# Kernel tuning notes

Hardware: AMD Instinct MI355X
Metric: run time of the kernel (lower is better)

The kernel has to match this reference:

```python
import jax, jax.numpy as jnp
import numpy as np

FAR = 10.0
RAST = 256          # rast_size default
ORIG_W, ORIG_H = 256.0, 256.0  # orig_size default
CHUNK = 32          # faces processed per scan step
EPS = 1e-9


def _project(vertices, K, R, t, dist):
    # persp projection with lens distortion; vertices [B,V,3] -> [B,V,3] (u,v in [-1,1], z depth)
    v = jnp.einsum('bvj,bij->bvi', vertices, R) + t
    x, y, z = v[..., 0], v[..., 1], v[..., 2]
    x_ = x / (z + EPS)
    y_ = y / (z + EPS)
    k1, k2, p1, p2, k3 = (dist[:, None, i] for i in range(5))
    r2 = x_ * x_ + y_ * y_  # == r**2 in original (r = sqrt(x_^2+y_^2))
    radial = 1.0 + k1 * r2 + k2 * r2 ** 2 + k3 * r2 ** 3
    x__ = x_ * radial + 2.0 * p1 * x_ * y_ + p2 * (r2 + 2.0 * x_ ** 2)
    y__ = y_ * radial + p1 * (r2 + 2.0 * y_ ** 2) + 2.0 * p2 * x_ * y_
    pts = jnp.stack([x__, y__, jnp.ones_like(z)], axis=-1)
    pts = jnp.einsum('bvj,bij->bvi', pts, K)
    u, vv = pts[..., 0], pts[..., 1]
    vv = ORIG_H - vv
    u = 2.0 * (u - ORIG_W / 2.0) / ORIG_W
    vv = 2.0 * (vv - ORIG_H / 2.0) / ORIG_H
    return jnp.stack([u, vv, z], axis=-1)


def _rasterize(fverts):
    # fverts: [B,F,3,3] per-face screen-space vertices (u,v,z). Z-buffer depth raster + coverage mask.
    B, F = fverts.shape[0], fverts.shape[1]
    pad = (-F) % CHUNK
    fv = jnp.pad(fverts, ((0, 0), (0, pad), (0, 0), (0, 0)))  # padded faces are degenerate (den==0)
    nc = (F + pad) // CHUNK
    fv = fv.reshape(B, nc, CHUNK, 3, 3).transpose(1, 0, 2, 3, 4)  # [nc,B,CHUNK,3,3]
    # pixel centers in [-1,1]; row i top-to-bottom maps to y = -1..1 (consistent with flipped v)
    g = 2.0 * (jnp.arange(RAST, dtype=jnp.float32) + 0.5) / RAST - 1.0
    X = g[None, None, None, :]   # cols
    Y = g[None, None, :, None]   # rows

    def body(carry, ch):
        zbuf, cover = carry
        e = lambda i, j: ch[:, :, i, j][:, :, None, None]
        ax, ay, az = e(0, 0), e(0, 1), e(0, 2)
        bx, by, bz = e(1, 0), e(1, 1), e(1, 2)
        cx, cy, cz = e(2, 0), e(2, 1), e(2, 2)
        den = (bx - ax) * (cy - ay) - (by - ay) * (cx - ax)
        ok = jnp.abs(den) > 1e-8
        den_s = jnp.where(ok, den, 1.0)
        # barycentric coords of each pixel wrt this face (signed; fill_back provides both windings)
        w0 = ((by - cy) * (X - cx) + (cx - bx) * (Y - cy)) / den_s
        w1 = ((cy - ay) * (X - cx) + (ax - cx) * (Y - cy)) / den_s
        w2 = 1.0 - w0 - w1
        zs = lambda zz: jnp.where(zz > 1e-8, zz, 1.0)
        inv = w0 / zs(az) + w1 / zs(bz) + w2 / zs(cz)  # perspective-correct 1/z interp
        valid = ok & (w0 >= 0) & (w1 >= 0) & (w2 >= 0)
        valid = valid & (az > 1e-8) & (bz > 1e-8) & (cz > 1e-8) & (inv > 1e-8)
        zp = 1.0 / jnp.where(valid, inv, 1.0)
        zc = jnp.min(jnp.where(valid, zp, FAR), axis=1)  # nearest face in this chunk [B,S,S]
        return (jnp.minimum(zbuf, zc), cover | jnp.any(valid, axis=1)), None

    zbuf0 = jnp.full((B, RAST, RAST), FAR, dtype=jnp.float32)
    cov0 = jnp.zeros((B, RAST, RAST), dtype=bool)
    (zbuf, cover), _ = jax.lax.scan(body, (zbuf0, cov0), fv)
    return zbuf, cover


def _normalize_depth(img, far):
    img_inf = (img == far).astype(jnp.float32)
    img_no_back = (1.0 - img_inf) * img
    img_max = img_no_back.max(axis=1, keepdims=True).max(axis=2, keepdims=True)
    img_min = img.min(axis=1, keepdims=True).min(axis=2, keepdims=True)
    nd = (img_max - img) / (img_max - img_min + 1e-4)
    return jnp.clip(nd, 0.0, 1.0)


def _forward(vertices, faces, intr, R, t, dist_coeffs):
    # fill_back=True: append faces with reversed vertex order
    faces_fb = jnp.concatenate([faces, faces[:, :, ::-1]], axis=1)
    uvz = _project(vertices, intr, R, t, dist_coeffs)
    fverts = jax.vmap(lambda v, f: v[f])(uvz, faces_fb)  # [B,F,3,3]
    zbuf, cover = _rasterize(fverts)
    dep = _normalize_depth(zbuf, FAR)
    mask = cover.astype(jnp.float32)
    return dep, mask


def setup_inputs():
    key = jax.random.key(0)
    k0, k1, k2 = jax.random.split(key, 3)
    B, V, F = 4, 778, 1538  # MANO hand mesh
    vertices = jax.random.normal(k0, (B, V, 3), dtype=jnp.float32) * 0.1 \
        + jnp.array([0.0, 0.0, 0.6], dtype=jnp.float32)  # blob 0.6m in front of camera
    faces = jax.random.randint(k1, (B, F, 3), 0, V, dtype=jnp.int32)
    K = jnp.tile(jnp.array([[500.0, 0.0, 128.0],
                            [0.0, 500.0, 128.0],
                            [0.0, 0.0, 1.0]], dtype=jnp.float32)[None], (B, 1, 1))
    R = jnp.tile(jnp.eye(3, dtype=jnp.float32)[None], (B, 1, 1))
    t = jnp.zeros((B, 1, 3), dtype=jnp.float32)
    dist_coeffs = jax.random.uniform(k2, (B, 5), dtype=jnp.float32) * 0.01
    return {"vertices": vertices, "faces": faces, "intr": K, "R": R, "t": t,
            "dist_coeffs": dist_coeffs}


def reference(vertices, faces, intr, R, t, dist_coeffs):
    return _forward(vertices, faces, intr, R, t, dist_coeffs)
```

## Files before the change

kernel.cpp:

```cpp
#include <hip/hip_runtime.h>
#include <cstdint>

#define RASTN 256
#define FARV 10.0f
#define FARBITS 0x41200000u
#define SPLIT 4
#define NBUCK 1024
#define NINITY 8

__device__ __forceinline__ float gval(int i) {
    return (2.0f * ((float)i + 0.5f)) / 256.0f - 1.0f;
}

__global__ __launch_bounds__(1024) void prep_sort_kernel(
    const float* __restrict__ verts, const int* __restrict__ faces,
    const float* __restrict__ Km, const float* __restrict__ Rm,
    const float* __restrict__ tm, const float* __restrict__ dm,
    float4* __restrict__ rec, uint2* __restrict__ sax, unsigned short* __restrict__ stri,
    unsigned int* __restrict__ zbits, unsigned int* __restrict__ mm,
    float* __restrict__ uvzg, int V, int F, int F2, int B, int npix)
{
#pragma clang fp contract(off)
    __shared__ float s_uvz[1024*3];
    __shared__ unsigned int s_pk[4096];
    __shared__ unsigned short s_bk[4096];
    __shared__ unsigned int s_hist[NBUCK], s_cnt2[NBUCK];
    __shared__ unsigned int s_ws[16];
    int b = blockIdx.x, y = blockIdx.y, tid = threadIdx.x;
    int lane = tid & 63, wv16 = tid >> 6;
    uint4* zb4 = (uint4*)(zbits + (size_t)b * npix);
    int n4 = npix >> 2;
    int sl0 = (n4 * y) / NINITY, sl1 = (n4 * (y + 1)) / NINITY;
    for (int i = sl0 + tid; i < sl1; i += 1024)
        zb4[i] = make_uint4(FARBITS, FARBITS, FARBITS, FARBITS);
    if (y > 0) return;
    if (tid == 0) { mm[2*b] = 0u; mm[2*b+1] = FARBITS; }
    for (int i = tid; i < NBUCK; i += 1024) s_hist[i] = 0u;
    bool inlds = (V <= 1024);
    const float* R = Rm + b*9; const float* K = Km + b*9;
    const float* t = tm + b*3; const float* d = dm + b*5;
    for (int v = tid; v < V; v += 1024) {
        float vx = verts[((size_t)b*V + v)*3+0];
        float vy = verts[((size_t)b*V + v)*3+1];
        float vz = verts[((size_t)b*V + v)*3+2];
        float cxm = ((vx*R[0] + vy*R[1]) + vz*R[2]) + t[0];
        float cym = ((vx*R[3] + vy*R[4]) + vz*R[5]) + t[1];
        float czm = ((vx*R[6] + vy*R[7]) + vz*R[8]) + t[2];
        float zd = czm + 1e-9f;
        float x_ = cxm / zd;
        float y_ = cym / zd;
        float k1 = d[0], k2 = d[1], p1 = d[2], p2 = d[3], k3 = d[4];
        float r2   = (x_*x_) + (y_*y_);
        float r2_2 = r2 * r2;
        float r2_3 = r2 * r2_2;
        float radial = ((1.0f + k1*r2) + k2*r2_2) + k3*r2_3;
        float x__ = ((x_*radial) + (((2.0f*p1)*x_)*y_)) + (p2*(r2 + 2.0f*(x_*x_)));
        float y__ = ((y_*radial) + (p1*(r2 + 2.0f*(y_*y_)))) + (((2.0f*p2)*x_)*y_);
        float up = ((x__*K[0]) + (y__*K[1])) + (1.0f*K[2]);
        float vp = ((x__*K[3]) + (y__*K[4])) + (1.0f*K[5]);
        vp = 256.0f - vp;
        float un = (2.0f*(up - 128.0f)) / 256.0f;
        float vn = (2.0f*(vp - 128.0f)) / 256.0f;
        if (inlds) { s_uvz[v*3+0]=un; s_uvz[v*3+1]=vn; s_uvz[v*3+2]=czm; }
        else { uvzg[((size_t)b*V+v)*3+0]=un; uvzg[((size_t)b*V+v)*3+1]=vn; uvzg[((size_t)b*V+v)*3+2]=czm; }
    }
    __syncthreads();
    const float* ub = inlds ? s_uvz : (uvzg + (size_t)b*V*3);
    const int* fb = faces + (size_t)b * F * 3;
    float4* rb = rec + (size_t)b * F2 * 4;
    bool stash = (F2 <= 4096);
    for (int j = tid; j < F2; j += 1024) {
        int i0, i1, i2;
        if (j < F) { i0 = fb[j*3+0]; i1 = fb[j*3+1]; i2 = fb[j*3+2]; }
        else { int jj = j - F; i0 = fb[jj*3+2]; i1 = fb[jj*3+1]; i2 = fb[jj*3+0]; }
        float ax = ub[i0*3+0], ay = ub[i0*3+1], az = ub[i0*3+2];
        float bx = ub[i1*3+0], by = ub[i1*3+1], bz = ub[i1*3+2];
        float cx = ub[i2*3+0], cy = ub[i2*3+1], cz = ub[i2*3+2];
        float den = (bx-ax)*(cy-ay) - (by-ay)*(cx-ax);
        bool ok = fabsf(den) > 1e-8f;
        float dens = ok ? den : 1.0f;
        bool alive = ok && (az > 1e-8f) && (bz > 1e-8f) && (cz > 1e-8f);
        float za = (az > 1e-8f) ? az : 1.0f;
        float zb = (bz > 1e-8f) ? bz : 1.0f;
        float zc = (cz > 1e-8f) ? cz : 1.0f;
        float mnx = fminf(ax, fminf(bx, cx));
        float mxx = fmaxf(ax, fmaxf(bx, cx));
        float mny = fminf(ay, fminf(by, cy));
        float mxy = fmaxf(ay, fmaxf(by, cy));
        float m = 1e-3f + 1e-6f*((fabsf(mnx)+fabsf(mxx))+(fabsf(mny)+fabsf(mxy)));
        mnx -= m; mxx += m; mny -= m; mxy += m;
        if (!(mxx >= -1.0f) || !(mnx <= 1.0f) || !(mxy >= -1.0f) || !(mny <= 1.0f)) alive = false;
        int ic0 = 1, ic1 = 0, ir0 = 1, ir1 = 0;
        float minz = 3e38f;
        if (alive) {
            float lx = fmaxf(mnx, -1.5f), hx = fminf(mxx, 1.5f);
            float ly = fmaxf(mny, -1.5f), hy = fminf(mxy, 1.5f);
            ic0 = (int)floorf((lx + 1.0f) * 128.0f - 0.5f);
            ic1 = (int)ceilf ((hx + 1.0f) * 128.0f - 0.5f);
            ir0 = (int)floorf((ly + 1.0f) * 128.0f - 0.5f);
            ir1 = (int)ceilf ((hy + 1.0f) * 128.0f - 0.5f);
            ic0 = ic0 < 0 ? 0 : ic0;  ir0 = ir0 < 0 ? 0 : ir0;
            ic1 = ic1 > 255 ? 255 : ic1;  ir1 = ir1 > 255 ? 255 : ir1;
            if (ic0 > ic1 || ir0 > ir1) { ic0 = 1; ic1 = 0; ir0 = 1; ir1 = 0; minz = 3e38f; }
            else minz = fminf(za, fminf(zb, zc)) * (1.0f - 4e-4f);
        }
        float minzv = fminf(za, fminf(zb, zc));
        float maxzv = fmaxf(za, fmaxf(zb, zc));
        float rd = __builtin_amdgcn_rcpf(dens);
        float ra, rbz, rc;
        if (minzv > 1e-2f && maxzv < 100.0f * minzv) {
            ra  = __builtin_amdgcn_rcpf(za);
            rbz = __builtin_amdgcn_rcpf(zb);
            rc  = __builtin_amdgcn_rcpf(zc);
        } else {
            ra = rbz = rc = __builtin_huge_valf();
        }
        unsigned int pack = (unsigned int)(ic0 | (ic1 << 8) | (ir0 << 16) | (ir1 << 24));
        int bk = NBUCK - 1;
        if (minz < 1e30f) {
            bk = (int)(minz * 512.0f);
            bk = bk < 0 ? 0 : (bk > NBUCK-2 ? NBUCK-2 : bk);
        }
        size_t base = (size_t)j * 4;
        rb[base+0] = make_float4(cx, cy, by - cy, cx - bx);
        rb[base+1] = make_float4(cy - ay, ax - cx, rd, ra);
        rb[base+2] = make_float4(dens, za, zb, zc);
        rb[base+3] = make_float4(__uint_as_float(pack), minz, rbz, rc);
        atomicAdd(&s_hist[bk], 1u);
        if (stash) { s_pk[j] = pack; s_bk[j] = (unsigned short)bk; }
    }
    __syncthreads();
    {
        unsigned int h = s_hist[tid];
        unsigned int v = h;
        for (int o = 1; o < 64; o <<= 1) {
            unsigned int tsh = __shfl_up(v, o, 64);
            if (lane >= o) v += tsh;
        }
        if (lane == 63) s_ws[wv16] = v;
        __syncthreads();
        if (tid < 16) {
            unsigned int w = s_ws[tid];
            for (int o = 1; o < 16; o <<= 1) {
                unsigned int tsh = __shfl_up(w, o, 64);
                if (tid >= o) w += tsh;
            }
            s_ws[tid] = w;
        }
        __syncthreads();
        unsigned int add = (wv16 > 0) ? s_ws[wv16 - 1] : 0u;
        s_cnt2[tid] = v + add - h;
    }
    __syncthreads();
    uint2* sxb = sax + (size_t)b * F2;
    unsigned short* stb = stri + (size_t)b * F2;
    for (int j = tid; j < F2; j += 1024) {
        unsigned int pack; int bk;
        if (stash) { pack = s_pk[j]; bk = (int)s_bk[j]; }
        else {
            float4 q3 = rb[(size_t)j*4+3];
            pack = __float_as_uint(q3.x);
            float mz = q3.y;
            bk = NBUCK - 1;
            if (mz < 1e30f) { bk = (int)(mz * 512.0f); bk = bk < 0 ? 0 : (bk > NBUCK-2 ? NBUCK-2 : bk); }
        }
        float key = (bk == NBUCK-1) ? 3e38f : (float)bk * (1.0f/512.0f);
        int pos = (int)atomicAdd(&s_cnt2[bk], 1u);
        sxb[pos] = make_uint2(pack, __float_as_uint(key));
        stb[pos] = (unsigned short)j;
    }
}

__global__ __launch_bounds__(256) void raster_kernel(
    const float4* __restrict__ rec, const uint2* __restrict__ sax,
    const unsigned short* __restrict__ stri, unsigned int* __restrict__ zbits,
    int F2)
{
#pragma clang fp contract(off)
    __shared__ float4 sh[2][256];
    __shared__ float2 s_mzbb[2][64];
    __shared__ unsigned short s_list[256];
    __shared__ int s_wk[4], s_kk[4], s_wo[4];
    __shared__ int s_tot, s_kc;
    __shared__ float s_tzmax, s_red[4];
    int zz = blockIdx.z;
    int b = zz / SPLIT, sp = zz - b*SPLIT;
    int tc = blockIdx.x, tr = blockIdx.y;
    int tid = threadIdx.x, lane = tid & 63, wv = tid >> 6;
    int tx = tid & 15, ty = tid >> 4;
    int col = tc*16 + tx, row = tr*16 + ty;
    float X = gval(col), Y = gval(row);
    int pc0 = tc*16, pc1 = pc0+15, pr0 = tr*16, pr1 = pr0+15;
    const float4* rb = rec + (size_t)b * F2 * 4;
    const uint2* sxb = sax + (size_t)b * F2;
    const unsigned short* stb = stri + (size_t)b * F2;
    size_t pix = ((size_t)b*RASTN + row)*RASTN + col;
    unsigned int* zp_g = zbits + pix;
    float zmin = FARV;
    float pushed = FARV;
    if (tid == 0) s_tzmax = FARV;
    __syncthreads();
    int nch = (F2 + 256*SPLIT - 1) / (256*SPLIT);
    for (int c = 0; c < nch; ++c) {
        int s = (c*256 + tid)*SPLIT + sp;
        bool kp = false, sv = false; unsigned int tri = 0;
        if (s < F2) {
            uint2 a = sxb[s];
            float kf = __uint_as_float(a.y);
            kp = !(kf > s_tzmax);
            if (kp) {
                int pk = (int)a.x;
                int ic0 = pk & 255, ic1 = (pk >> 8) & 255;
                int ir0 = (pk >> 16) & 255, ir1 = (pk >> 24) & 255;
                sv = (ic0 <= ic1) && (ic0 <= pc1) && (ic1 >= pc0) && (ir0 <= pr1) && (ir1 >= pr0);
                if (sv) tri = stb[s];
            }
        }
        unsigned long long bs = __ballot(sv ? 1 : 0);
        unsigned long long bk = __ballot(kp ? 1 : 0);
        int pfx = __popcll(bs & ((1ull << lane) - 1ull));
        if (lane == 0) { s_wk[wv] = __popcll(bs); s_kk[wv] = __popcll(bk); }
        __syncthreads();
        if (tid == 0) {
            int acc = 0;
            for (int q = 0; q < 4; ++q) { s_wo[q] = acc; acc += s_wk[q]; }
            s_tot = acc;
            s_kc = s_kk[0] + s_kk[1] + s_kk[2] + s_kk[3];
        }
        __syncthreads();
        if (sv) s_list[s_wo[wv] + pfx] = (unsigned short)tri;
        int kcnt = s_kc, n = s_tot;
        if (kcnt == 0) break;
        float zg = __uint_as_float(__hip_atomic_load(
            zp_g, __ATOMIC_RELAXED, __HIP_MEMORY_SCOPE_AGENT));
        __syncthreads();
        int ngrp = (n + 63) >> 6;
        if (n > 0) {
            int cnt0 = n < 64 ? n : 64;
            if (tid < cnt0*4) {
                unsigned int t4 = s_list[tid >> 2];
                float4 f = rb[(size_t)t4*4 + (tid & 3)];
                sh[0][tid] = f;
                if ((tid & 3) == 3) s_mzbb[0][tid >> 2] = make_float2(f.y, f.x);
            }
        }
        __syncthreads();
        for (int gi = 0; gi < ngrp; ++gi) {
            int buf = gi & 1;
            pushed = fminf(pushed, zg);
            zmin = fminf(zmin, zg);
            float zg_n = __uint_as_float(__hip_atomic_load(
                zp_g, __ATOMIC_RELAXED, __HIP_MEMORY_SCOPE_AGENT));
            float4 fpref = make_float4(0.f, 0.f, 0.f, 0.f);
            bool hp = false;
            if (gi + 1 < ngrp) {
                int g2 = (gi + 1) << 6;
                int cnt3 = (n - g2) < 64 ? (n - g2) : 64;
                if (tid < cnt3*4) {
                    unsigned int t4 = s_list[g2 + (tid >> 2)];
                    fpref = rb[(size_t)t4*4 + (tid & 3)];
                    hp = true;
                }
            }
            int g = gi << 6;
            int cnt2 = (n - g) < 64 ? (n - g) : 64;
            float2 nx = s_mzbb[buf][0];
            for (int i = 0; i < cnt2; ++i) {
                float mz = nx.x;
                int pk = __float_as_int(nx.y);
                nx = s_mzbb[buf][(i + 1) & 63];
                if (mz > zmin) continue;
                int ic0 = pk & 255, ic1 = (pk >> 8) & 255;
                int ir0 = (pk >> 16) & 255, ir1 = (pk >> 24) & 255;
                if (col < ic0 || col > ic1 || row < ir0 || row > ir1) continue;
                float4 q0 = sh[buf][i*4+0];
                float4 q1 = sh[buf][i*4+1];
                float xc = X - q0.x;
                float yc = Y - q0.y;
                float e0 = (q0.z*xc) + (q0.w*yc);
                float e1 = (q1.x*xc) + (q1.y*yc);
                float rd = q1.z;
                float sgn = copysignf(1.0f, rd);
                float s0 = e0*sgn, s1 = e1*sgn;
                float w0a = e0*rd, w1a = e1*rd;
                float w2a = (1.0f - w0a) - w1a;
                float epsu = 1e-4f*((1.0f + fabsf(w0a)) + fabsf(w1a));
                if (s0 > -1e-30f && s1 > -1e-30f && w2a > -epsu) {
                    float4 q3 = sh[buf][i*4+3];
                    float inva = ((w0a*q1.w) + (w1a*q3.z)) + (w2a*q3.w);
                    float zpa = __builtin_amdgcn_rcpf(inva);
                    bool clearly = (s0 > 0.0f) && (s1 > 0.0f) && (w2a > epsu) && (inva > 1e-6f);
                    if (!clearly || zpa < zmin*1.001f) {
                        float4 q2 = sh[buf][i*4+2];
                        float dens = q2.x;
                        float w0 = e0 / dens;
                        float w1 = e1 / dens;
                        float w2 = (1.0f - w0) - w1;
                        float inv = ((w0 / q2.y) + (w1 / q2.z)) + (w2 / q2.w);
                        if ((w0 >= 0.0f) && (w1 >= 0.0f) && (w2 >= 0.0f) && (inv > 1e-8f)) {
                            float zp = 1.0f / inv;
                            zmin = fminf(zmin, zp);
                        }
                    }
                }
            }
            if (zmin < pushed) {
                atomicMin(zp_g, __float_as_uint(zmin));
                pushed = zmin;
            }
            zg = zg_n;
            if (hp) {
                sh[buf ^ 1][tid] = fpref;
                if ((tid & 3) == 3) s_mzbb[buf ^ 1][tid >> 2] = make_float2(fpref.y, fpref.x);
            }
            __syncthreads();
        }
        if (n > 0) {
            float zx = zmin;
            for (int o = 32; o; o >>= 1) zx = fmaxf(zx, __shfl_xor(zx, o));
            if (lane == 0) s_red[wv] = zx;
        }
        __syncthreads();
        if (n > 0 && tid == 0)
            s_tzmax = fminf(s_tzmax,
                fmaxf(fmaxf(s_red[0], s_red[1]), fmaxf(s_red[2], s_red[3])));
        __syncthreads();
    }
    if (zmin < pushed)
        atomicMin(zp_g, __float_as_uint(zmin));
}

__global__ __launch_bounds__(256) void minmax_kernel(
    const float4* __restrict__ zbuf, float4* __restrict__ mask,
    unsigned int* __restrict__ mm, int npix)
{
    __shared__ float smx[4], smn[4];
    int b = blockIdx.y;
    size_t i4 = (((size_t)b * npix) >> 2) + (size_t)blockIdx.x * 256 + threadIdx.x;
    float4 z = zbuf[i4];
    float4 mk;
    mk.x = (z.x < FARV) ? 1.0f : 0.0f;
    mk.y = (z.y < FARV) ? 1.0f : 0.0f;
    mk.z = (z.z < FARV) ? 1.0f : 0.0f;
    mk.w = (z.w < FARV) ? 1.0f : 0.0f;
    mask[i4] = mk;
    float nbx = (z.x == FARV) ? 0.0f : z.x;
    float nby = (z.y == FARV) ? 0.0f : z.y;
    float nbz = (z.z == FARV) ? 0.0f : z.z;
    float nbw = (z.w == FARV) ? 0.0f : z.w;
    float vmx = fmaxf(fmaxf(nbx, nby), fmaxf(nbz, nbw));
    float vmn = fminf(fminf(z.x, z.y), fminf(z.z, z.w));
    int lane = threadIdx.x & 63, wv = threadIdx.x >> 6;
    for (int o = 32; o; o >>= 1) {
        vmx = fmaxf(vmx, __shfl_xor(vmx, o));
        vmn = fminf(vmn, __shfl_xor(vmn, o));
    }
    if (lane == 0) { smx[wv] = vmx; smn[wv] = vmn; }
    __syncthreads();
    if (threadIdx.x == 0) {
        float bmx = fmaxf(fmaxf(smx[0], smx[1]), fmaxf(smx[2], smx[3]));
        float bmn = fminf(fminf(smn[0], smn[1]), fminf(smn[2], smn[3]));
        atomicMax(mm + 2*b,     __float_as_uint(bmx));
        atomicMin(mm + 2*b + 1, __float_as_uint(bmn));
    }
}

__global__ __launch_bounds__(256) void final_kernel(
    float4* __restrict__ zdep, const unsigned int* __restrict__ mm,
    int npix4, int total4)
{
#pragma clang fp contract(off)
    int idx = blockIdx.x*256 + threadIdx.x;
    if (idx >= total4) return;
    int b = idx / npix4;
    float mx = __uint_as_float(mm[2*b]);
    float mn = __uint_as_float(mm[2*b + 1]);
    float den = (mx - mn) + 1e-4f;
    float4 z = zdep[idx];
    float4 r;
    r.x = (mx - z.x) / den;
    r.y = (mx - z.y) / den;
    r.z = (mx - z.z) / den;
    r.w = (mx - z.w) / den;
    r.x = r.x < 0.0f ? 0.0f : (r.x > 1.0f ? 1.0f : r.x);
    r.y = r.y < 0.0f ? 0.0f : (r.y > 1.0f ? 1.0f : r.y);
    r.z = r.z < 0.0f ? 0.0f : (r.z > 1.0f ? 1.0f : r.z);
    r.w = r.w < 0.0f ? 0.0f : (r.w > 1.0f ? 1.0f : r.w);
    zdep[idx] = r;
}

extern "C" void kernel_launch(void* const* d_in, const int* in_sizes, int n_in,
                              void* d_out, int out_size, void* d_ws, size_t ws_size,
                              hipStream_t stream)
{
    const float* verts = (const float*)d_in[0];
    const int*   faces = (const int*)d_in[1];
    const float* Km    = (const float*)d_in[2];
    const float* Rm    = (const float*)d_in[3];
    const float* tm    = (const float*)d_in[4];
    const float* dm    = (const float*)d_in[5];
    float* out = (float*)d_out;

    int B  = in_sizes[2] / 9;
    int V  = in_sizes[0] / (3 * B);
    int F  = in_sizes[1] / (3 * B);
    int F2 = 2 * F;
    int npix = RASTN * RASTN;

    char* ws = (char*)d_ws;
    size_t off = 0;
    float4* rec = (float4*)(ws + off);
    off = (off + (size_t)B * F2 * 4 * sizeof(float4) + 255) & ~(size_t)255;
    uint2* sax = (uint2*)(ws + off);
    off = (off + (size_t)B * F2 * sizeof(uint2) + 255) & ~(size_t)255;
    unsigned short* stri = (unsigned short*)(ws + off);
    off = (off + (size_t)B * F2 * sizeof(unsigned short) + 255) & ~(size_t)255;
    float* uvzg = (float*)(ws + off);
    off = (off + (size_t)B * V * 3 * sizeof(float) + 255) & ~(size_t)255;
    unsigned int* mm = (unsigned int*)(ws + off);

    unsigned int* zbits = (unsigned int*)out;
    float* mask = out + (size_t)B * npix;

    dim3 pgrid(B, NINITY);
    prep_sort_kernel<<<pgrid, 1024, 0, stream>>>(
        verts, faces, Km, Rm, tm, dm, rec, sax, stri, zbits, mm, uvzg,
        V, F, F2, B, npix);
    dim3 rgrid(16, 16, B * SPLIT);
    raster_kernel<<<rgrid, 256, 0, stream>>>(rec, sax, stri, zbits, F2);
    dim3 mgrid(npix / 1024, B);
    minmax_kernel<<<mgrid, 256, 0, stream>>>(
        (const float4*)zbits, (float4*)mask, mm, npix);
    int npix4 = npix >> 2;
    int total4 = B * npix4;
    final_kernel<<<(total4 + 255) / 256, 256, 0, stream>>>(
        (float4*)zbits, mm, npix4, total4);
}
```

Measured before the change: 182.1 us.

## Fuse minmax into raster via last-block tile counter, add edge-function tile culling

```diff
diff --git a/kernel.cpp b/kernel.cpp
--- a/kernel.cpp
+++ b/kernel.cpp
@@ -18,6 +18,7 @@
     const float* __restrict__ tm, const float* __restrict__ dm,
     float4* __restrict__ rec, uint2* __restrict__ sax, unsigned short* __restrict__ stri,
     unsigned int* __restrict__ zbits, unsigned int* __restrict__ mm,
+    unsigned int* __restrict__ tilecnt,
     float* __restrict__ uvzg, int V, int F, int F2, int B, int npix)
 {
 #pragma clang fp contract(off)
@@ -35,6 +36,7 @@
         zb4[i] = make_uint4(FARBITS, FARBITS, FARBITS, FARBITS);
     if (y > 0) return;
     if (tid == 0) { mm[2*b] = 0u; mm[2*b+1] = FARBITS; }
+    for (int i = tid; i < 256; i += 1024) tilecnt[b*256 + i] = 0u;
     for (int i = tid; i < NBUCK; i += 1024) s_hist[i] = 0u;
     bool inlds = (V <= 1024);
     const float* R = Rm + b*9; const float* K = Km + b*9;
@@ -174,15 +176,17 @@
 __global__ __launch_bounds__(256) void raster_kernel(
     const float4* __restrict__ rec, const uint2* __restrict__ sax,
     const unsigned short* __restrict__ stri, unsigned int* __restrict__ zbits,
-    int F2)
+    float* __restrict__ mask, unsigned int* __restrict__ mm,
+    unsigned int* __restrict__ tilecnt, int F2)
 {
 #pragma clang fp contract(off)
-    __shared__ float4 sh[2][256];
-    __shared__ float2 s_mzbb[2][64];
+    __shared__ float4 sh[256];
+    __shared__ int s_bb[64];
+    __shared__ float s_key[256];
     __shared__ unsigned short s_list[256];
     __shared__ int s_wk[4], s_kk[4], s_wo[4];
-    __shared__ int s_tot, s_kc;
-    __shared__ float s_tzmax, s_red[4];
+    __shared__ int s_tot, s_kc, s_done;
+    __shared__ float s_tzmax, s_red[4], s_red2[4];
     int zz = blockIdx.z;
     int b = zz / SPLIT, sp = zz - b*SPLIT;
     int tc = blockIdx.x, tr = blockIdx.y;
@@ -191,6 +195,10 @@
     int col = tc*16 + tx, row = tr*16 + ty;
     float X = gval(col), Y = gval(row);
     int pc0 = tc*16, pc1 = pc0+15, pr0 = tr*16, pr1 = pr0+15;
+    int wr0 = pr0 + wv*4, wr1 = wr0 + 3;
+    float Xc = 0.5f*(gval(pc0) + gval(pc1));
+    float Yc = 0.5f*(gval(pr0) + gval(pr1));
+    const float hxr = 15.0f/256.0f, hyr = 15.0f/256.0f;
     const float4* rb = rec + (size_t)b * F2 * 4;
     const uint2* sxb = sax + (size_t)b * F2;
     const unsigned short* stb = stri + (size_t)b * F2;
@@ -203,17 +211,41 @@
     int nch = (F2 + 256*SPLIT - 1) / (256*SPLIT);
     for (int c = 0; c < nch; ++c) {
         int s = (c*256 + tid)*SPLIT + sp;
-        bool kp = false, sv = false; unsigned int tri = 0;
+        bool kp = false, sv = false; unsigned int tri = 0; float kf = 0.0f;
         if (s < F2) {
             uint2 a = sxb[s];
-            float kf = __uint_as_float(a.y);
+            kf = __uint_as_float(a.y);
             kp = !(kf > s_tzmax);
             if (kp) {
                 int pk = (int)a.x;
                 int ic0 = pk & 255, ic1 = (pk >> 8) & 255;
                 int ir0 = (pk >> 16) & 255, ir1 = (pk >> 24) & 255;
                 sv = (ic0 <= ic1) && (ic0 <= pc1) && (ic1 >= pc0) && (ir0 <= pr1) && (ir1 >= pr0);
-                if (sv) tri = stb[s];
+                if (sv) {
+                    tri = stb[s];
+                    float4 q0 = rb[(size_t)tri*4 + 0];
+                    float4 q1 = rb[(size_t)tri*4 + 1];
+                    float4 q2 = rb[(size_t)tri*4 + 2];
+                    float a0 = q0.z, b0 = q0.w;
+                    float a1 = q1.x, b1 = q1.y;
+                    float xcd = Xc - q0.x, ycd = Yc - q0.y;
+                    float e0c = (a0*xcd) + (b0*ycd);
+                    float e1c = (a1*xcd) + (b1*ycd);
+                    float den = q2.x;
+                    float e2c = (den - e0c) - e1c;
+                    float a2 = -(a0 + a1), b2 = -(b0 + b1);
+                    float sg = copysignf(1.0f, den);
+                    float t0 = fabsf(a0)*hxr + fabsf(b0)*hyr;
+                    float t1 = fabsf(a1)*hxr + fabsf(b1)*hyr;
+                    float t2 = fabsf(a2)*hxr + fabsf(b2)*hyr;
+                    float m0 = sg*e0c + t0;
+                    float m1 = sg*e1c + t1;
+                    float m2 = sg*e2c + t2;
+                    bool cull = (m0 < -1e-5f*(fabsf(e0c) + t0 + 1.0f))
+                             || (m1 < -1e-5f*(fabsf(e1c) + t1 + 1.0f))
+                             || (m2 < -1e-5f*(fabsf(e2c) + t2 + 1.0f));
+                    if (cull) sv = false;
+                }
             }
         }
         unsigned long long bs = __ballot(sv ? 1 : 0);
@@ -228,53 +260,39 @@
             s_kc = s_kk[0] + s_kk[1] + s_kk[2] + s_kk[3];
         }
         __syncthreads();
-        if (sv) s_list[s_wo[wv] + pfx] = (unsigned short)tri;
+        if (sv) {
+            int pos = s_wo[wv] + pfx;
+            s_list[pos] = (unsigned short)tri;
+            s_key[pos] = kf;
+        }
         int kcnt = s_kc, n = s_tot;
         if (kcnt == 0) break;
-        float zg = __uint_as_float(__hip_atomic_load(
-            zp_g, __ATOMIC_RELAXED, __HIP_MEMORY_SCOPE_AGENT));
-        __syncthreads();
-        int ngrp = (n + 63) >> 6;
-        if (n > 0) {
-            int cnt0 = n < 64 ? n : 64;
-            if (tid < cnt0*4) {
-                unsigned int t4 = s_list[tid >> 2];
+        for (int g = 0; g < n; g += 64) {
+            __syncthreads();
+            int cnt2 = (n - g) < 64 ? (n - g) : 64;
+            if (tid < cnt2*4) {
+                unsigned int t4 = s_list[g + (tid >> 2)];
                 float4 f = rb[(size_t)t4*4 + (tid & 3)];
-                sh[0][tid] = f;
-                if ((tid & 3) == 3) s_mzbb[0][tid >> 2] = make_float2(f.y, f.x);
-            }
-        }
-        __syncthreads();
-        for (int gi = 0; gi < ngrp; ++gi) {
-            int buf = gi & 1;
-            pushed = fminf(pushed, zg);
-            zmin = fminf(zmin, zg);
-            float zg_n = __uint_as_float(__hip_atomic_load(
-                zp_g, __ATOMIC_RELAXED, __HIP_MEMORY_SCOPE_AGENT));
-            float4 fpref = make_float4(0.f, 0.f, 0.f, 0.f);
-            bool hp = false;
-            if (gi + 1 < ngrp) {
-                int g2 = (gi + 1) << 6;
-                int cnt3 = (n - g2) < 64 ? (n - g2) : 64;
-                if (tid < cnt3*4) {
-                    unsigned int t4 = s_list[g2 + (tid >> 2)];
-                    fpref = rb[(size_t)t4*4 + (tid & 3)];
-                    hp = true;
-                }
-            }
-            int g = gi << 6;
-            int cnt2 = (n - g) < 64 ? (n - g) : 64;
-            float2 nx = s_mzbb[buf][0];
+                sh[tid] = f;
+                if ((tid & 3) == 3) s_bb[tid >> 2] = __float_as_int(f.x);
+            }
+            __syncthreads();
+            {
+                float zg = __uint_as_float(__hip_atomic_load(
+                    zp_g, __ATOMIC_RELAXED, __HIP_MEMORY_SCOPE_AGENT));
+                pushed = fminf(pushed, zg);
+                zmin = fminf(zmin, zg);
+            }
             for (int i = 0; i < cnt2; ++i) {
-                float mz = nx.x;
-                int pk = __float_as_int(nx.y);
-                nx = s_mzbb[buf][(i + 1) & 63];
-                if (mz > zmin) continue;
+                float ky = s_key[g + i];
+                if (ky > zmin) break;
+                int pk = s_bb[i];
+                int ir0 = (pk >> 16) & 255, ir1 = (pk >> 24) & 255;
+                if (ir1 < wr0 || ir0 > wr1) continue;
                 int ic0 = pk & 255, ic1 = (pk >> 8) & 255;
-                int ir0 = (pk >> 16) & 255, ir1 = (pk >> 24) & 255;
                 if (col < ic0 || col > ic1 || row < ir0 || row > ir1) continue;
-                float4 q0 = sh[buf][i*4+0];
-                float4 q1 = sh[buf][i*4+1];
+                float4 q0 = sh[i*4+0];
+                float4 q1 = sh[i*4+1];
                 float xc = X - q0.x;
                 float yc = Y - q0.y;
                 float e0 = (q0.z*xc) + (q0.w*yc);
@@ -286,12 +304,12 @@
                 float w2a = (1.0f - w0a) - w1a;
                 float epsu = 1e-4f*((1.0f + fabsf(w0a)) + fabsf(w1a));
                 if (s0 > -1e-30f && s1 > -1e-30f && w2a > -epsu) {
-                    float4 q3 = sh[buf][i*4+3];
+                    float4 q3 = sh[i*4+3];
                     float inva = ((w0a*q1.w) + (w1a*q3.z)) + (w2a*q3.w);
                     float zpa = __builtin_amdgcn_rcpf(inva);
                     bool clearly = (s0 > 0.0f) && (s1 > 0.0f) && (w2a > epsu) && (inva > 1e-6f);
                     if (!clearly || zpa < zmin*1.001f) {
-                        float4 q2 = sh[buf][i*4+2];
+                        float4 q2 = sh[i*4+2];
                         float dens = q2.x;
                         float w0 = e0 / dens;
                         float w1 = e1 / dens;
@@ -308,12 +326,6 @@
                 atomicMin(zp_g, __float_as_uint(zmin));
                 pushed = zmin;
             }
-            zg = zg_n;
-            if (hp) {
-                sh[buf ^ 1][tid] = fpref;
-                if ((tid & 3) == 3) s_mzbb[buf ^ 1][tid >> 2] = make_float2(fpref.y, fpref.x);
-            }
-            __syncthreads();
         }
         if (n > 0) {
             float zx = zmin;
@@ -328,40 +340,32 @@
     }
     if (zmin < pushed)
         atomicMin(zp_g, __float_as_uint(zmin));
-}
-
-__global__ __launch_bounds__(256) void minmax_kernel(
-    const float4* __restrict__ zbuf, float4* __restrict__ mask,
-    unsigned int* __restrict__ mm, int npix)
-{
-    __shared__ float smx[4], smn[4];
-    int b = blockIdx.y;
-    size_t i4 = (((size_t)b * npix) >> 2) + (size_t)blockIdx.x * 256 + threadIdx.x;
-    float4 z = zbuf[i4];
-    float4 mk;
-    mk.x = (z.x < FARV) ? 1.0f : 0.0f;
-    mk.y = (z.y < FARV) ? 1.0f : 0.0f;
-    mk.z = (z.z < FARV) ? 1.0f : 0.0f;
-    mk.w = (z.w < FARV) ? 1.0f : 0.0f;
-    mask[i4] = mk;
-    float nbx = (z.x == FARV) ? 0.0f : z.x;
-    float nby = (z.y == FARV) ? 0.0f : z.y;
-    float nbz = (z.z == FARV) ? 0.0f : z.z;
-    float nbw = (z.w == FARV) ? 0.0f : z.w;
-    float vmx = fmaxf(fmaxf(nbx, nby), fmaxf(nbz, nbw));
-    float vmn = fminf(fminf(z.x, z.y), fminf(z.z, z.w));
-    int lane = threadIdx.x & 63, wv = threadIdx.x >> 6;
-    for (int o = 32; o; o >>= 1) {
-        vmx = fmaxf(vmx, __shfl_xor(vmx, o));
-        vmn = fminf(vmn, __shfl_xor(vmn, o));
-    }
-    if (lane == 0) { smx[wv] = vmx; smn[wv] = vmn; }
-    __syncthreads();
-    if (threadIdx.x == 0) {
-        float bmx = fmaxf(fmaxf(smx[0], smx[1]), fmaxf(smx[2], smx[3]));
-        float bmn = fminf(fminf(smn[0], smn[1]), fminf(smn[2], smn[3]));
-        atomicMax(mm + 2*b,     __float_as_uint(bmx));
-        atomicMin(mm + 2*b + 1, __float_as_uint(bmn));
+    __threadfence();
+    __syncthreads();
+    if (tid == 0)
+        s_done = (int)__hip_atomic_fetch_add(
+            &tilecnt[(size_t)b*256 + tr*16 + tc], 1u,
+            __ATOMIC_ACQ_REL, __HIP_MEMORY_SCOPE_AGENT);
+    __syncthreads();
+    if (s_done == SPLIT-1) {
+        __threadfence();
+        float z = __uint_as_float(__hip_atomic_load(
+            zp_g, __ATOMIC_RELAXED, __HIP_MEMORY_SCOPE_AGENT));
+        mask[pix] = (z < FARV) ? 1.0f : 0.0f;
+        float nb = (z == FARV) ? 0.0f : z;
+        float vmx = nb, vmn = z;
+        for (int o = 32; o; o >>= 1) {
+            vmx = fmaxf(vmx, __shfl_xor(vmx, o));
+            vmn = fminf(vmn, __shfl_xor(vmn, o));
+        }
+        if (lane == 0) { s_red[wv] = vmx; s_red2[wv] = vmn; }
+        __syncthreads();
+        if (tid == 0) {
+            float bmx = fmaxf(fmaxf(s_red[0], s_red[1]), fmaxf(s_red[2], s_red[3]));
+            float bmn = fminf(fminf(s_red2[0], s_red2[1]), fminf(s_red2[2], s_red2[3]));
+            atomicMax(mm + 2*b,     __float_as_uint(bmx));
+            atomicMin(mm + 2*b + 1, __float_as_uint(bmn));
+        }
     }
 }
 
@@ -418,19 +422,18 @@
     float* uvzg = (float*)(ws + off);
     off = (off + (size_t)B * V * 3 * sizeof(float) + 255) & ~(size_t)255;
     unsigned int* mm = (unsigned int*)(ws + off);
+    unsigned int* tilecnt = mm + 2 * B;
 
     unsigned int* zbits = (unsigned int*)out;
     float* mask = out + (size_t)B * npix;
 
     dim3 pgrid(B, NINITY);
     prep_sort_kernel<<<pgrid, 1024, 0, stream>>>(
-        verts, faces, Km, Rm, tm, dm, rec, sax, stri, zbits, mm, uvzg,
+        verts, faces, Km, Rm, tm, dm, rec, sax, stri, zbits, mm, tilecnt, uvzg,
         V, F, F2, B, npix);
     dim3 rgrid(16, 16, B * SPLIT);
-    raster_kernel<<<rgrid, 256, 0, stream>>>(rec, sax, stri, zbits, F2);
-    dim3 mgrid(npix / 1024, B);
-    minmax_kernel<<<mgrid, 256, 0, stream>>>(
-        (const float4*)zbits, (float4*)mask, mm, npix);
+    raster_kernel<<<rgrid, 256, 0, stream>>>(
+        rec, sax, stri, zbits, mask, mm, tilecnt, F2);
     int npix4 = npix >> 2;
     int total4 = B * npix4;
     final_kernel<<<(total4 + 255) / 256, 256, 0, stream>>>(
```

After: 504.7 us. 2.77x slower.
